# Optimization experiments

Measured on AMD Instinct MI355X. Metric: run time of the kernel, lower is better.

## Reference

```python
import jax, jax.numpy as jnp
import numpy as np

B, FAN_IN, FAN_OUT, K = 4096, 4096, 4096, 65536


def setup_inputs() -> dict:
    key = jax.random.key(0)
    k1, k2, k3 = jax.random.split(key, 3)
    a = jax.random.normal(k1, (B, FAN_IN), dtype=jnp.float32)
    # hash table H(i, j) -> bucket k in [0, K); replaces the python defaultdict hh
    hash_idx = jax.random.randint(k2, (FAN_OUT, FAN_IN + 1), 0, K)
    d = FAN_OUT * (FAN_IN + 1) / K  # matches d = fan_out * fan_in / K (fan_in already +1)
    W = jax.random.normal(k3, (K,), dtype=jnp.float32) / d
    return {"a": a, "hash_idx": hash_idx, "W": W}


def reference(a, hash_idx, W):
    # append bias column of ones: a_ext [B, fan_in+1]
    ones = jnp.ones((a.shape[0], 1), dtype=a.dtype)
    a_ext = jnp.concatenate([a, ones], axis=1)
    # virtual weight matrix via hash gather: Wv[i, j] = W[H(i, j)]
    Wv = W[hash_idx]  # [fan_out, fan_in+1]
    # out[b, i] = sum_j a_ext[b, j] * W[H(i, j)]
    # identical math to: a_kj[i,b,k] = sum_{j: H(i,j)=k} a_ext[b,j]; zz = a_kj @ W; zz.T
    return jnp.einsum('bj,ij->bi', a_ext, Wv)
```

## Files before the change

kernel.cpp:

```cpp
#include <hip/hip_runtime.h>
#include <hip/hip_bf16.h>
#include <stdint.h>


#define B_DIM   4096
#define FAN_IN  4096
#define FAN_OUT 4096
#define KD      (FAN_IN + 1)
#define KP      4160
#define NKT     65

#define BM 256
#define BN 256
#define BK 64

typedef __attribute__((ext_vector_type(8))) short  short8;
typedef __attribute__((ext_vector_type(4))) float  floatx4;

__device__ __forceinline__ unsigned short f2bf(float f) {
  union { float f; unsigned u; } v; v.f = f;
  unsigned u = v.u;
  u += 0x7fffu + ((u >> 16) & 1u);
  return (unsigned short)(u >> 16);
}

__device__ __forceinline__ void async16(const void* g, void* l) {
  __builtin_amdgcn_global_load_lds(
      (const __attribute__((address_space(1))) void*)g,
      (__attribute__((address_space(3))) void*)l, 16, 0, 0);
}

__global__ __launch_bounds__(256) void build_aext(
    const float* __restrict__ a, unsigned short* __restrict__ Ae) {
  const int row = blockIdx.x;
  const float* ar = a + (size_t)row * FAN_IN;
  unsigned short* er = Ae + (size_t)row * KP;
  for (int j4 = threadIdx.x; j4 < KP / 4; j4 += 256) {
    const int j = j4 * 4;
    float x0, x1, x2, x3;
    if (j + 3 < FAN_IN) {
      const float4 v = *(const float4*)(ar + j);
      x0 = v.x; x1 = v.y; x2 = v.z; x3 = v.w;
    } else {
      x0 = (j + 0 < FAN_IN) ? ar[j + 0] : ((j + 0 == FAN_IN) ? 1.0f : 0.0f);
      x1 = (j + 1 < FAN_IN) ? ar[j + 1] : ((j + 1 == FAN_IN) ? 1.0f : 0.0f);
      x2 = (j + 2 < FAN_IN) ? ar[j + 2] : ((j + 2 == FAN_IN) ? 1.0f : 0.0f);
      x3 = (j + 3 < FAN_IN) ? ar[j + 3] : ((j + 3 == FAN_IN) ? 1.0f : 0.0f);
    }
    ushort4 o;
    o.x = f2bf(x0); o.y = f2bf(x1); o.z = f2bf(x2); o.w = f2bf(x3);
    *(ushort4*)(er + j) = o;
  }
}

__global__ __launch_bounds__(1024) void build_wv(
    const int* __restrict__ hidx, const float* __restrict__ W,
    unsigned short* __restrict__ Wv) {
  extern __shared__ unsigned short wl[];
  const int t = threadIdx.x;

  const float4* Wf = (const float4*)W;
#pragma unroll
  for (int i = 0; i < 16; i++) {
    const int f4 = i * 1024 + t;
    const float4 v = Wf[f4];
    ushort4 o;
    o.x = f2bf(v.x); o.y = f2bf(v.y); o.z = f2bf(v.z); o.w = f2bf(v.w);
    *(ushort4*)&wl[f4 * 4] = o;
  }
  __syncthreads();

  const int r0 = blockIdx.x * 16;
#pragma unroll 4
  for (int r = 0; r < 16; r++) {
    const int* hr = hidx + (size_t)(r0 + r) * KD;
    unsigned short* wr = Wv + (size_t)(r0 + r) * KP;
    const int j = 4 * t;
    ushort4 o;
    o.x = wl[hr[j + 0]];
    o.y = wl[hr[j + 1]];
    o.z = wl[hr[j + 2]];
    o.w = wl[hr[j + 3]];
    *(ushort4*)(wr + j) = o;
    if (t < 64)
      wr[4096 + t] = (t == 0) ? wl[hr[4096]] : (unsigned short)0;
  }
}


#define STAGE_A(BUF, H, KOFF)                                                      \
  do {                                                                             \
    async16(pa + ((H) * 128 + 0)  * KP + (KOFF),                                   \
            smb + ((BUF) << 15) + ((H) << 14) + dA);                               \
    async16(pa + ((H) * 128 + 64) * KP + (KOFF),                                   \
            smb + ((BUF) << 15) + ((H) << 14) + 8192 + dA);                        \
  } while (0)

#define STAGE_B(BUF, H, KOFF)                                                      \
  do {                                                                             \
    async16(pb + ((H) * 128 + 0)  * KP + (KOFF),                                   \
            smb + 65536 + ((BUF) << 15) + ((H) << 14) + dA);                       \
    async16(pb + ((H) * 128 + 64) * KP + (KOFF),                                   \
            smb + 65536 + ((BUF) << 15) + ((H) << 14) + 8192 + dA);                \
  } while (0)

#define PHASE_MID()                                                                \
  do {                                                                             \
    asm volatile("" ::: "memory");                                                 \
    __builtin_amdgcn_s_barrier();                                                  \
    asm volatile("s_waitcnt lgkmcnt(0)" ::: "memory");                             \
    __builtin_amdgcn_sched_barrier(0);                                             \
    __builtin_amdgcn_s_setprio(1);                                                 \
  } while (0)

#define PHASE_END()                                                                \
  do {                                                                             \
    __builtin_amdgcn_s_setprio(0);                                                 \
    asm volatile("" ::: "memory");                                                 \
    __builtin_amdgcn_s_barrier();                                                  \
    asm volatile("" ::: "memory");                                                 \
  } while (0)

#define PHASE_END_VM4()                                                            \
  do {                                                                             \
    __builtin_amdgcn_s_setprio(0);                                                 \
    asm volatile("s_waitcnt vmcnt(4)" ::: "memory");                               \
    __builtin_amdgcn_s_barrier();                                                  \
    asm volatile("" ::: "memory");                                                 \
  } while (0)

#define MFMA2(ACC, AF, BF)                                                         \
  do {                                                                             \
    ACC = __builtin_amdgcn_mfma_f32_16x16x32_bf16((AF)[0], (BF)[0], ACC, 0, 0, 0); \
    ACC = __builtin_amdgcn_mfma_f32_16x16x32_bf16((AF)[1], (BF)[1], ACC, 0, 0, 0); \
  } while (0)

#define KTILE(P, K2)                                                               \
  do {                                                                             \
    short8 af[4][2], bf[2][2];                                                     \
                      \
    PHASE_MID();                                                                   \
    _Pragma("unroll")                                                              \
    for (int mi = 0; mi < 4; ++mi)                                                 \
      _Pragma("unroll")                                                            \
      for (int ni = 0; ni < 2; ++ni) MFMA2(acc[mi][ni], afp[mi], bfp[ni]);         \
    PHASE_END();                                                                   \
                                  \
    _Pragma("unroll")                                                              \
    for (int ni = 0; ni < 2; ++ni) {                                               \
      bf[ni][0] = *(const short8*)(smb + ((P) << 15) + brB + (ni + 2) * 2048 + abase); \
      bf[ni][1] = *(const short8*)(smb + ((P) << 15) + brB + (ni + 2) * 2048 + (abase ^ 64)); \
    }                                                                              \
    PHASE_MID();                                                                   \
    _Pragma("unroll")                                                              \
    for (int mi = 0; mi < 4; ++mi)                                                 \
      _Pragma("unroll")                                                            \
      for (int ni = 0; ni < 2; ++ni) MFMA2(acc[mi][ni + 2], afp[mi], bf[ni]);      \
    PHASE_END();                                                                   \
        \
    _Pragma("unroll")                                                              \
    for (int mi = 0; mi < 4; ++mi) {                                               \
      af[mi][0] = *(const short8*)(smb + ((P) << 15) + arB + (mi + 4) * 2048 + abase); \
      af[mi][1] = *(const short8*)(smb + ((P) << 15) + arB + (mi + 4) * 2048 + (abase ^ 64)); \
    }                                                                              \
    STAGE_B((P), 0, K2);                                                           \
    STAGE_B((P), 1, K2);                                                           \
    PHASE_MID();                                                                   \
    _Pragma("unroll")                                                              \
    for (int mi = 0; mi < 4; ++mi)                                                 \
      _Pragma("unroll")                                                            \
      for (int ni = 0; ni < 2; ++ni) MFMA2(acc[mi + 4][ni], af[mi], bfp[ni]);      \
    PHASE_END_VM4();                \
          \
          \
                                                             \
    STAGE_A((P), 0, K2);                                                           \
    STAGE_A((P), 1, K2);                                                           \
    PHASE_MID();                                                                   \
    _Pragma("unroll")                                                              \
    for (int mi = 0; mi < 4; ++mi) {                                               \
      afp[mi][0] = *(const short8*)(smb + (((P) ^ 1) << 15) + arB + mi * 2048 + abase); \
      afp[mi][1] = *(const short8*)(smb + (((P) ^ 1) << 15) + arB + mi * 2048 + (abase ^ 64)); \
    }                                                                              \
    _Pragma("unroll")                                                              \
    for (int ni = 0; ni < 2; ++ni) {                                               \
      bfp[ni][0] = *(const short8*)(smb + (((P) ^ 1) << 15) + brB + ni * 2048 + abase); \
      bfp[ni][1] = *(const short8*)(smb + (((P) ^ 1) << 15) + brB + ni * 2048 + (abase ^ 64)); \
    }                                                                              \
    _Pragma("unroll")                                                              \
    for (int mi = 0; mi < 4; ++mi)                                                 \
      _Pragma("unroll")                                                            \
      for (int ni = 0; ni < 2; ++ni) MFMA2(acc[mi + 4][ni + 2], af[mi], bf[ni]);   \
    PHASE_END();                         \
  } while (0)

__global__ __launch_bounds__(512, 2) void gemm_bt8(
    const unsigned short* __restrict__ A, const unsigned short* __restrict__ Bm,
    float* __restrict__ C, int M, int N) {
  extern __shared__ char smb[];
  const int tid = threadIdx.x;
  const int l   = tid & 63;
  const int w   = tid >> 6;
  const int wm  = w >> 2;
  const int wn  = w & 3;
  const int bm  = blockIdx.y * BM;
  const int bn  = blockIdx.x * BN;
  const int q   = l >> 4;
  const int r   = l & 15;

  const int lrow = l >> 3;
  const int lcol = ((l & 7) ^ lrow) * 8;
  const unsigned short* pa = A  + (size_t)(bm + w * 8 + lrow) * KP + lcol;
  const unsigned short* pb = Bm + (size_t)(bn + w * 8 + lrow) * KP + lcol;
  const int dA = w * 1024;

  const int abase = r * 128 + ((q ^ (r & 7)) << 4);
  const int arB   = wm << 14;
  const int brB   = 65536 + ((wn >> 1) << 14) + ((wn & 1) << 13);

  floatx4 acc[8][4] = {};
  short8 afp[4][2], bfp[2][2];

  STAGE_A(0, 0, 0); STAGE_A(0, 1, 0);
  STAGE_B(0, 0, 0); STAGE_B(0, 1, 0);
  STAGE_B(1, 0, 64); STAGE_B(1, 1, 64);
  STAGE_A(1, 0, 64); STAGE_A(1, 1, 64);
  asm volatile("s_waitcnt vmcnt(8)" ::: "memory");
  __builtin_amdgcn_s_barrier();
  asm volatile("" ::: "memory");
#pragma unroll
  for (int mi = 0; mi < 4; ++mi) {
    afp[mi][0] = *(const short8*)(smb + arB + mi * 2048 + abase);
    afp[mi][1] = *(const short8*)(smb + arB + mi * 2048 + (abase ^ 64));
  }
#pragma unroll
  for (int ni = 0; ni < 2; ++ni) {
    bfp[ni][0] = *(const short8*)(smb + brB + ni * 2048 + abase);
    bfp[ni][1] = *(const short8*)(smb + brB + ni * 2048 + (abase ^ 64));
  }

  int k2 = 128;
#pragma unroll 1
  for (int tt = 0; tt < 32; ++tt) {
    const int k3c = (k2 + 64 > 4096) ? 4096 : k2 + 64;
    KTILE(0, k2);
    KTILE(1, k3c);
    k2 += 128;
  }

  {
    short8 aft[4][2], bft[2][2];
#pragma unroll
    for (int mi = 0; mi < 4; ++mi) {
      aft[mi][0] = *(const short8*)(smb + arB + (mi + 4) * 2048 + abase);
      aft[mi][1] = *(const short8*)(smb + arB + (mi + 4) * 2048 + (abase ^ 64));
    }
#pragma unroll
    for (int ni = 0; ni < 2; ++ni) {
      bft[ni][0] = *(const short8*)(smb + brB + (ni + 2) * 2048 + abase);
      bft[ni][1] = *(const short8*)(smb + brB + (ni + 2) * 2048 + (abase ^ 64));
    }
    asm volatile("s_waitcnt lgkmcnt(0)" ::: "memory");
    __builtin_amdgcn_sched_barrier(0);
    __builtin_amdgcn_s_setprio(1);
#pragma unroll
    for (int mi = 0; mi < 4; ++mi)
#pragma unroll
      for (int ni = 0; ni < 2; ++ni) {
        MFMA2(acc[mi][ni],          afp[mi], bfp[ni]);
        MFMA2(acc[mi][ni + 2],      afp[mi], bft[ni]);
        MFMA2(acc[mi + 4][ni],      aft[mi], bfp[ni]);
        MFMA2(acc[mi + 4][ni + 2],  aft[mi], bft[ni]);
      }
    __builtin_amdgcn_s_setprio(0);
  }

  asm volatile("s_waitcnt vmcnt(0)" ::: "memory");

  const int r0 = bm + wm * 128;
  const int c0 = bn + wn * 64;
#pragma unroll
  for (int mi = 0; mi < 8; ++mi)
#pragma unroll
    for (int ni = 0; ni < 4; ++ni) {
      const int row0 = r0 + mi * 16 + q * 4;
      const int col  = c0 + ni * 16 + r;
#pragma unroll
      for (int i = 0; i < 4; ++i)
        C[(size_t)(row0 + i) * N + col] = acc[mi][ni][i];
    }
}

extern "C" void kernel_launch(void* const* d_in, const int* in_sizes, int n_in,
                              void* d_out, int out_size, void* d_ws, size_t ws_size,
                              hipStream_t stream) {
  const float* a    = (const float*)d_in[0];
  const int*   hidx = (const int*)d_in[1];
  const float* W    = (const float*)d_in[2];
  float*       out  = (float*)d_out;

  unsigned short* Ae = (unsigned short*)d_ws;
  unsigned short* Wv = Ae + (size_t)B_DIM * KP;

  static bool attr_set = false;
  if (!attr_set) {
    hipFuncSetAttribute((const void*)gemm_bt8,
                        hipFuncAttributeMaxDynamicSharedMemorySize, 131072);
    hipFuncSetAttribute((const void*)build_wv,
                        hipFuncAttributeMaxDynamicSharedMemorySize, 131072);
    attr_set = true;
  }

  build_aext<<<B_DIM, 256, 0, stream>>>(a, Ae);
  build_wv<<<FAN_OUT / 16, 1024, 131072, stream>>>(hidx, W, Wv);
  gemm_bt8<<<dim3(FAN_OUT / BN, B_DIM / BM), 512, 131072, stream>>>(Ae, Wv, out, B_DIM, FAN_OUT);
}
```

Baseline: 288.6 us.

## Fuse prep kernels and GEMM into one persistent kernel with grid barrier

Merges the bf16 conversion of activations, the hashed weight gather, and the GEMM into a single launch of 256 blocks. Each block first builds 16 rows of Wv and 16 rows of Ae, then all blocks meet at a software grid barrier on a global atomic counter before the GEMM starts. This is meant to remove two kernel launches and the gaps between them. In exchange it relies on all 256 blocks being co-resident, since the spin-wait could deadlock otherwise. The prep phases now run at only 256 blocks of 512 threads, and each block reloads the whole 64K-entry W table into LDS.

```diff
diff --git a/kernel.cpp b/kernel.cpp
--- a/kernel.cpp
+++ b/kernel.cpp
@@ -17,6 +17,8 @@
 typedef __attribute__((ext_vector_type(8))) short  short8;
 typedef __attribute__((ext_vector_type(4))) float  floatx4;
 
+__device__ unsigned int g_sync_cnt = 0;
+
 __device__ __forceinline__ unsigned short f2bf(float f) {
   union { float f; unsigned u; } v; v.f = f;
   unsigned u = v.u;
@@ -28,63 +30,6 @@
   __builtin_amdgcn_global_load_lds(
       (const __attribute__((address_space(1))) void*)g,
       (__attribute__((address_space(3))) void*)l, 16, 0, 0);
-}
-
-__global__ __launch_bounds__(256) void build_aext(
-    const float* __restrict__ a, unsigned short* __restrict__ Ae) {
-  const int row = blockIdx.x;
-  const float* ar = a + (size_t)row * FAN_IN;
-  unsigned short* er = Ae + (size_t)row * KP;
-  for (int j4 = threadIdx.x; j4 < KP / 4; j4 += 256) {
-    const int j = j4 * 4;
-    float x0, x1, x2, x3;
-    if (j + 3 < FAN_IN) {
-      const float4 v = *(const float4*)(ar + j);
-      x0 = v.x; x1 = v.y; x2 = v.z; x3 = v.w;
-    } else {
-      x0 = (j + 0 < FAN_IN) ? ar[j + 0] : ((j + 0 == FAN_IN) ? 1.0f : 0.0f);
-      x1 = (j + 1 < FAN_IN) ? ar[j + 1] : ((j + 1 == FAN_IN) ? 1.0f : 0.0f);
-      x2 = (j + 2 < FAN_IN) ? ar[j + 2] : ((j + 2 == FAN_IN) ? 1.0f : 0.0f);
-      x3 = (j + 3 < FAN_IN) ? ar[j + 3] : ((j + 3 == FAN_IN) ? 1.0f : 0.0f);
-    }
-    ushort4 o;
-    o.x = f2bf(x0); o.y = f2bf(x1); o.z = f2bf(x2); o.w = f2bf(x3);
-    *(ushort4*)(er + j) = o;
-  }
-}
-
-__global__ __launch_bounds__(1024) void build_wv(
-    const int* __restrict__ hidx, const float* __restrict__ W,
-    unsigned short* __restrict__ Wv) {
-  extern __shared__ unsigned short wl[];
-  const int t = threadIdx.x;
-
-  const float4* Wf = (const float4*)W;
-#pragma unroll
-  for (int i = 0; i < 16; i++) {
-    const int f4 = i * 1024 + t;
-    const float4 v = Wf[f4];
-    ushort4 o;
-    o.x = f2bf(v.x); o.y = f2bf(v.y); o.z = f2bf(v.z); o.w = f2bf(v.w);
-    *(ushort4*)&wl[f4 * 4] = o;
-  }
-  __syncthreads();
-
-  const int r0 = blockIdx.x * 16;
-#pragma unroll 4
-  for (int r = 0; r < 16; r++) {
-    const int* hr = hidx + (size_t)(r0 + r) * KD;
-    unsigned short* wr = Wv + (size_t)(r0 + r) * KP;
-    const int j = 4 * t;
-    ushort4 o;
-    o.x = wl[hr[j + 0]];
-    o.y = wl[hr[j + 1]];
-    o.z = wl[hr[j + 2]];
-    o.w = wl[hr[j + 3]];
-    *(ushort4*)(wr + j) = o;
-    if (t < 64)
-      wr[4096 + t] = (t == 0) ? wl[hr[4096]] : (unsigned short)0;
-  }
 }
 
 
@@ -172,8 +117,7 @@
       for (int ni = 0; ni < 2; ++ni) MFMA2(acc[mi + 4][ni], af[mi], bfp[ni]);      \
     PHASE_END_VM4();                \
           \
-          \
-                                                             \
+                                              \
     STAGE_A((P), 0, K2);                                                           \
     STAGE_A((P), 1, K2);                                                           \
     PHASE_MID();                                                                   \
@@ -194,101 +138,172 @@
     PHASE_END();                         \
   } while (0)
 
-__global__ __launch_bounds__(512, 2) void gemm_bt8(
-    const unsigned short* __restrict__ A, const unsigned short* __restrict__ Bm,
-    float* __restrict__ C, int M, int N) {
+__global__ __launch_bounds__(512, 2) void fused(
+    const float* __restrict__ a, const int* __restrict__ hidx,
+    const float* __restrict__ W, unsigned short* __restrict__ Ae,
+    unsigned short* __restrict__ Wv, float* __restrict__ C) {
   extern __shared__ char smb[];
   const int tid = threadIdx.x;
-  const int l   = tid & 63;
-  const int w   = tid >> 6;
-  const int wm  = w >> 2;
-  const int wn  = w & 3;
-  const int bm  = blockIdx.y * BM;
-  const int bn  = blockIdx.x * BN;
-  const int q   = l >> 4;
-  const int r   = l & 15;
-
-  const int lrow = l >> 3;
-  const int lcol = ((l & 7) ^ lrow) * 8;
-  const unsigned short* pa = A  + (size_t)(bm + w * 8 + lrow) * KP + lcol;
-  const unsigned short* pb = Bm + (size_t)(bn + w * 8 + lrow) * KP + lcol;
-  const int dA = w * 1024;
-
-  const int abase = r * 128 + ((q ^ (r & 7)) << 4);
-  const int arB   = wm << 14;
-  const int brB   = 65536 + ((wn >> 1) << 14) + ((wn & 1) << 13);
-
-  floatx4 acc[8][4] = {};
-  short8 afp[4][2], bfp[2][2];
-
-  STAGE_A(0, 0, 0); STAGE_A(0, 1, 0);
-  STAGE_B(0, 0, 0); STAGE_B(0, 1, 0);
-  STAGE_B(1, 0, 64); STAGE_B(1, 1, 64);
-  STAGE_A(1, 0, 64); STAGE_A(1, 1, 64);
-  asm volatile("s_waitcnt vmcnt(8)" ::: "memory");
-  __builtin_amdgcn_s_barrier();
-  asm volatile("" ::: "memory");
-#pragma unroll
-  for (int mi = 0; mi < 4; ++mi) {
-    afp[mi][0] = *(const short8*)(smb + arB + mi * 2048 + abase);
-    afp[mi][1] = *(const short8*)(smb + arB + mi * 2048 + (abase ^ 64));
-  }
-#pragma unroll
-  for (int ni = 0; ni < 2; ++ni) {
-    bfp[ni][0] = *(const short8*)(smb + brB + ni * 2048 + abase);
-    bfp[ni][1] = *(const short8*)(smb + brB + ni * 2048 + (abase ^ 64));
-  }
-
-  int k2 = 128;
+  const int lin = blockIdx.y * 16 + blockIdx.x;
+  const int r0p = lin * 16;
+
+  {
+    unsigned short* wl = (unsigned short*)smb;
+    const float4* Wf = (const float4*)W;
+#pragma unroll
+    for (int i = 0; i < 32; i++) {
+      const int f4 = i * 512 + tid;
+      const float4 v = Wf[f4];
+      ushort4 o;
+      o.x = f2bf(v.x); o.y = f2bf(v.y); o.z = f2bf(v.z); o.w = f2bf(v.w);
+      *(ushort4*)&wl[f4 * 4] = o;
+    }
+    __syncthreads();
+
+#pragma unroll 2
+    for (int r = 0; r < 16; r++) {
+      const int* hr = hidx + (size_t)(r0p + r) * KD;
+      unsigned short* wr = Wv + (size_t)(r0p + r) * KP;
+      const int j = 8 * tid;
+      short8 o;
+#pragma unroll
+      for (int k = 0; k < 8; k++) o[k] = (short)wl[hr[j + k]];
+      *(short8*)(wr + j) = o;
+      if (tid < 64)
+        wr[4096 + tid] = (tid == 0) ? wl[hr[4096]] : (unsigned short)0;
+    }
+  }
+
+  for (int rr = 0; rr < 16; rr++) {
+    const int row = r0p + rr;
+    const float* ar = a + (size_t)row * FAN_IN;
+    unsigned short* er = Ae + (size_t)row * KP;
+    for (int j4 = tid; j4 < KP / 4; j4 += 512) {
+      const int j = j4 * 4;
+      float x0, x1, x2, x3;
+      if (j + 3 < FAN_IN) {
+        const float4 v = *(const float4*)(ar + j);
+        x0 = v.x; x1 = v.y; x2 = v.z; x3 = v.w;
+      } else {
+        x0 = (j + 0 < FAN_IN) ? ar[j + 0] : ((j + 0 == FAN_IN) ? 1.0f : 0.0f);
+        x1 = (j + 1 < FAN_IN) ? ar[j + 1] : ((j + 1 == FAN_IN) ? 1.0f : 0.0f);
+        x2 = (j + 2 < FAN_IN) ? ar[j + 2] : ((j + 2 == FAN_IN) ? 1.0f : 0.0f);
+        x3 = (j + 3 < FAN_IN) ? ar[j + 3] : ((j + 3 == FAN_IN) ? 1.0f : 0.0f);
+      }
+      ushort4 o;
+      o.x = f2bf(x0); o.y = f2bf(x1); o.z = f2bf(x2); o.w = f2bf(x3);
+      *(ushort4*)(er + j) = o;
+    }
+  }
+
+  __threadfence();
+  __syncthreads();
+  if (tid == 0) {
+    const unsigned gen = atomicAdd(&g_sync_cnt, 1u);
+    const unsigned target = ((gen >> 8) + 1u) << 8;
+    while (__hip_atomic_load(&g_sync_cnt, __ATOMIC_RELAXED,
+                             __HIP_MEMORY_SCOPE_AGENT) < target) {
+      __builtin_amdgcn_s_sleep(8);
+    }
+  }
+  __syncthreads();
+  __threadfence();
+
+  {
+    const unsigned short* A  = Ae;
+    const unsigned short* Bm = Wv;
+    const int N = FAN_OUT;
+    const int l   = tid & 63;
+    const int w   = tid >> 6;
+    const int wm  = w >> 2;
+    const int wn  = w & 3;
+    const int bm  = blockIdx.y * BM;
+    const int bn  = blockIdx.x * BN;
+    const int q   = l >> 4;
+    const int r   = l & 15;
+
+    const int lrow = l >> 3;
+    const int lcol = ((l & 7) ^ lrow) * 8;
+    const unsigned short* pa = A  + (size_t)(bm + w * 8 + lrow) * KP + lcol;
+    const unsigned short* pb = Bm + (size_t)(bn + w * 8 + lrow) * KP + lcol;
+    const int dA = w * 1024;
+
+    const int abase = r * 128 + ((q ^ (r & 7)) << 4);
+    const int arB   = wm << 14;
+    const int brB   = 65536 + ((wn >> 1) << 14) + ((wn & 1) << 13);
+
+    floatx4 acc[8][4] = {};
+    short8 afp[4][2], bfp[2][2];
+
+    STAGE_A(0, 0, 0); STAGE_A(0, 1, 0);
+    STAGE_B(0, 0, 0); STAGE_B(0, 1, 0);
+    STAGE_B(1, 0, 64); STAGE_B(1, 1, 64);
+    STAGE_A(1, 0, 64); STAGE_A(1, 1, 64);
+    asm volatile("s_waitcnt vmcnt(8)" ::: "memory");
+    __builtin_amdgcn_s_barrier();
+    asm volatile("" ::: "memory");
+#pragma unroll
+    for (int mi = 0; mi < 4; ++mi) {
+      afp[mi][0] = *(const short8*)(smb + arB + mi * 2048 + abase);
+      afp[mi][1] = *(const short8*)(smb + arB + mi * 2048 + (abase ^ 64));
+    }
+#pragma unroll
+    for (int ni = 0; ni < 2; ++ni) {
+      bfp[ni][0] = *(const short8*)(smb + brB + ni * 2048 + abase);
+      bfp[ni][1] = *(const short8*)(smb + brB + ni * 2048 + (abase ^ 64));
+    }
+
+    int k2 = 128;
 #pragma unroll 1
-  for (int tt = 0; tt < 32; ++tt) {
-    const int k3c = (k2 + 64 > 4096) ? 4096 : k2 + 64;
-    KTILE(0, k2);
-    KTILE(1, k3c);
-    k2 += 128;
-  }
-
-  {
-    short8 aft[4][2], bft[2][2];
-#pragma unroll
-    for (int mi = 0; mi < 4; ++mi) {
-      aft[mi][0] = *(const short8*)(smb + arB + (mi + 4) * 2048 + abase);
-      aft[mi][1] = *(const short8*)(smb + arB + (mi + 4) * 2048 + (abase ^ 64));
-    }
-#pragma unroll
-    for (int ni = 0; ni < 2; ++ni) {
-      bft[ni][0] = *(const short8*)(smb + brB + (ni + 2) * 2048 + abase);
-      bft[ni][1] = *(const short8*)(smb + brB + (ni + 2) * 2048 + (abase ^ 64));
-    }
-    asm volatile("s_waitcnt lgkmcnt(0)" ::: "memory");
-    __builtin_amdgcn_sched_barrier(0);
-    __builtin_amdgcn_s_setprio(1);
-#pragma unroll
-    for (int mi = 0; mi < 4; ++mi)
+    for (int tt = 0; tt < 32; ++tt) {
+      const int k3c = (k2 + 64 > 4096) ? 4096 : k2 + 64;
+      KTILE(0, k2);
+      KTILE(1, k3c);
+      k2 += 128;
+    }
+
+    {
+      short8 aft[4][2], bft[2][2];
+#pragma unroll
+      for (int mi = 0; mi < 4; ++mi) {
+        aft[mi][0] = *(const short8*)(smb + arB + (mi + 4) * 2048 + abase);
+        aft[mi][1] = *(const short8*)(smb + arB + (mi + 4) * 2048 + (abase ^ 64));
+      }
 #pragma unroll
       for (int ni = 0; ni < 2; ++ni) {
-        MFMA2(acc[mi][ni],          afp[mi], bfp[ni]);
-        MFMA2(acc[mi][ni + 2],      afp[mi], bft[ni]);
-        MFMA2(acc[mi + 4][ni],      aft[mi], bfp[ni]);
-        MFMA2(acc[mi + 4][ni + 2],  aft[mi], bft[ni]);
+        bft[ni][0] = *(const short8*)(smb + brB + (ni + 2) * 2048 + abase);
+        bft[ni][1] = *(const short8*)(smb + brB + (ni + 2) * 2048 + (abase ^ 64));
       }
-    __builtin_amdgcn_s_setprio(0);
-  }
-
-  asm volatile("s_waitcnt vmcnt(0)" ::: "memory");
-
-  const int r0 = bm + wm * 128;
-  const int c0 = bn + wn * 64;
-#pragma unroll
-  for (int mi = 0; mi < 8; ++mi)
-#pragma unroll
-    for (int ni = 0; ni < 4; ++ni) {
-      const int row0 = r0 + mi * 16 + q * 4;
-      const int col  = c0 + ni * 16 + r;
-#pragma unroll
-      for (int i = 0; i < 4; ++i)
-        C[(size_t)(row0 + i) * N + col] = acc[mi][ni][i];
-    }
+      asm volatile("s_waitcnt lgkmcnt(0)" ::: "memory");
+      __builtin_amdgcn_sched_barrier(0);
+      __builtin_amdgcn_s_setprio(1);
+#pragma unroll
+      for (int mi = 0; mi < 4; ++mi)
+#pragma unroll
+        for (int ni = 0; ni < 2; ++ni) {
+          MFMA2(acc[mi][ni],          afp[mi], bfp[ni]);
+          MFMA2(acc[mi][ni + 2],      afp[mi], bft[ni]);
+          MFMA2(acc[mi + 4][ni],      aft[mi], bfp[ni]);
+          MFMA2(acc[mi + 4][ni + 2],  aft[mi], bft[ni]);
+        }
+      __builtin_amdgcn_s_setprio(0);
+    }
+
+    asm volatile("s_waitcnt vmcnt(0)" ::: "memory");
+
+    const int r0 = bm + wm * 128;
+    const int c0 = bn + wn * 64;
+#pragma unroll
+    for (int mi = 0; mi < 8; ++mi)
+#pragma unroll
+      for (int ni = 0; ni < 4; ++ni) {
+        const int row0 = r0 + mi * 16 + q * 4;
+        const int col  = c0 + ni * 16 + r;
+#pragma unroll
+        for (int i = 0; i < 4; ++i)
+          C[(size_t)(row0 + i) * N + col] = acc[mi][ni][i];
+      }
+  }
 }
 
 extern "C" void kernel_launch(void* const* d_in, const int* in_sizes, int n_in,
@@ -304,14 +319,11 @@
 
   static bool attr_set = false;
   if (!attr_set) {
-    hipFuncSetAttribute((const void*)gemm_bt8,
-                        hipFuncAttributeMaxDynamicSharedMemorySize, 131072);
-    hipFuncSetAttribute((const void*)build_wv,
+    hipFuncSetAttribute((const void*)fused,
                         hipFuncAttributeMaxDynamicSharedMemorySize, 131072);
     attr_set = true;
   }
 
-  build_aext<<<B_DIM, 256, 0, stream>>>(a, Ae);
-  build_wv<<<FAN_OUT / 16, 1024, 131072, stream>>>(hidx, W, Wv);
-  gemm_bt8<<<dim3(FAN_OUT / BN, B_DIM / BM), 512, 131072, stream>>>(Ae, Wv, out, B_DIM, FAN_OUT);
+  fused<<<dim3(FAN_OUT / BN, B_DIM / BM), 512, 131072, stream>>>(
+      a, hidx, W, Ae, Wv, out);
 }
```

Measured after the change: 392.6 us. 1.36x slower.
